# Performance work log

Hardware: AMD Instinct MI355X
Metric: run time of the kernel (lower is better)

The kernel has to match this reference:

```python
import jax, jax.numpy as jnp
from jax import lax
import numpy as np

N_BINS = 8
SIGMA = (1.0, 2.0)
ALPHA = (1.0, 2.0, 4.0)
BETA = (0.02, 0.05)
KSIZE = 7
BOUNDS = (0.0, 1.0)
C, H, W = 3, 512, 512


def gaussian_kernel(size, s):
    # matches torch: linspace(-size//2+1, size//2, size) == arange(size)-size//2 for odd size
    x = jnp.arange(size, dtype=jnp.float32) - size // 2
    g = jnp.exp(-(x[:, None] ** 2 + x[None, :] ** 2) / (2.0 * s ** 2))
    return g / jnp.sum(g)


def setup_inputs() -> dict:
    key = jax.random.key(0)
    im_th = jax.random.uniform(key, (H, W, C), dtype=jnp.float32)
    sks = max(3, int(SIGMA[-1] * 4))
    if sks % 2 == 0:
        sks += 1
    sigma_kernels = jnp.stack([gaussian_kernel(sks, s) for s in SIGMA])      # (S, Ks, Ks)
    alpha_kernels = jnp.stack([gaussian_kernel(KSIZE, a) for a in ALPHA])    # (A, k, k)
    edges = jnp.linspace(BOUNDS[0], BOUNDS[1], N_BINS + 1, dtype=jnp.float32)
    bin_centers = (edges[1:] + edges[:-1]) / 2.0                             # (N,)
    betas = jnp.array(BETA, dtype=jnp.float32)                               # (B,)
    return dict(im_th=im_th, sigma_kernels=sigma_kernels,
                alpha_kernels=alpha_kernels, bin_centers=bin_centers, betas=betas)


def _conv_per_channel(x, k):
    # x: (M, H, W); k: (K, kh, kw) -> (M, K, H, W). Channels treated as batch,
    # equivalent to torch grouped conv with groups=M and K kernels per group.
    p = k.shape[-1] // 2
    return lax.conv_general_dilated(x[:, None], k[:, None], (1, 1),
                                    [(p, p), (p, p)],
                                    dimension_numbers=('NCHW', 'OIHW', 'NCHW'))


def reference(im_th, sigma_kernels, alpha_kernels, bin_centers, betas):
    x = jnp.clip(im_th, 0.0, 1.0).transpose(2, 0, 1)  # (C, H, W)
    C_, H_, W_ = x.shape
    S = sigma_kernels.shape[0]
    A = alpha_kernels.shape[0]
    B = betas.shape[0]
    N = bin_centers.shape[0]
    # per-channel blur at each sigma: (C, S, H, W)
    conv = _conv_per_channel(x, sigma_kernels)
    # gaussian soft-binning: (B, N, C, S, H, W)
    diff = conv[None, None] - bin_centers[None, :, None, None, None, None]
    bv = betas[:, None, None, None, None, None]
    iso = jnp.exp(-0.5 * (diff / bv) ** 2) / (jnp.sqrt(2.0 * jnp.pi) * bv)
    # depthwise alpha aggregation over all B*N*C*S channels: (M, A, H, W)
    out = _conv_per_channel(iso.reshape(B * N * C_ * S, H_, W_), alpha_kernels)
    loi = out.reshape(B, N, C_, S, A, H_, W_).transpose(4, 0, 3, 2, 5, 6, 1)
    return loi  # (A, B, S, C, H, W, N)
```

## Files before the change

### kernel.cpp

```cpp
#include <hip/hip_runtime.h>

#define IMH 512
#define IMW 512

#define SM_OFF   0
#define IMT_OFF  560
#define SVT_OFF  1616
#define ISO_OFF  560
#define VV_OFF   4816

__global__ __launch_bounds__(256) void loi_fused(
    const float* __restrict__ im,
    const float* __restrict__ sigk,
    const float* __restrict__ alphak,
    const float* __restrict__ binc,
    const float* __restrict__ betas,
    float* __restrict__ out)
{
  const int t     = threadIdx.x;
  const int combo = blockIdx.z;
  const int b     = combo / 6;
  const int sc    = combo % 6;
  const int s     = sc / 3;
  const int c     = sc % 3;
  const int tx0   = blockIdx.x * 32;
  const int ty0   = blockIdx.y * 8;

  __shared__ __align__(16) float smem[12112];
  __shared__ float kf[3][8];
  __shared__ float sf[12];

  float* imt = smem + IMT_OFF;
  float* svt = smem + SVT_OFF;
  float* smt = smem + SM_OFF;

  for (int e = t; e < 1056; e += 256) {
    int j = e / 48, i = e - j * 48;
    float v = 0.f;
    if (i < 46) {
      int gy = ty0 + j - 7, gx = tx0 + i - 7;
      if (gy >= 0 && gy < IMH && gx >= 0 && gx < IMW) {
        v = im[(gy * IMW + gx) * 3 + c];
        v = fminf(fmaxf(v, 0.f), 1.f);
      }
    }
    imt[e] = v;
  }
  if (t < 9) {
    float acc = 0.f;
    #pragma unroll
    for (int j = 0; j < 9; j++) acc += sigk[s * 81 + t * 9 + j];
    sf[t] = acc;
  }
  if (t >= 32 && t < 56) {
    int a = (t - 32) >> 3, d = t & 7;
    float v = 0.f;
    if (d < 7) {
      #pragma unroll
      for (int j = 0; j < 7; j++) v += alphak[a * 49 + d * 7 + j];
    }
    kf[a][d] = v;
  }
  __syncthreads();

  for (int e = t; e < 672; e += 256) {
    int rr = e / 48, i = e - rr * 48;
    if (i < 46) {
      float acc = 0.f;
      #pragma unroll
      for (int d = 0; d < 9; d++) acc = fmaf(sf[d], imt[(rr + d) * 48 + i], acc);
      svt[e] = acc;
    }
  }
  __syncthreads();

  for (int e = t; e < 560; e += 256) {
    int rr = e / 40, j = e - rr * 40;
    if (j < 38) {
      float acc = 0.f;
      #pragma unroll
      for (int d = 0; d < 9; d++) acc = fmaf(sf[d], svt[rr * 48 + j + d], acc);
      smt[e] = acc;
    }
  }
  __syncthreads();

  const float beta = betas[b];
  const float norm = 0.39894228040143268f / beta;
  const float c2   = -0.72134752044448170f / (beta * beta);
  const float ctr  = binc[t & 7];
  float* iso = smem + ISO_OFF;
  for (int e = t; e < 4256; e += 256) {
    int q  = e >> 3;
    int rr = q / 38, jj = q - rr * 38;
    float v  = smt[rr * 40 + jj];
    float tt = v - ctr;
    float E  = exp2f(tt * tt * c2) * norm;
    int X = tx0 + jj - 3, Y = ty0 + rr - 3;
    bool valid = ((unsigned)X < IMW) && ((unsigned)Y < IMH);
    iso[e] = valid ? E : 0.f;
  }
  __syncthreads();

  float k0[7], k1[7], k2[7];
  #pragma unroll
  for (int d = 0; d < 7; d++) {
    k0[d] = kf[0][d];
    k1[d] = kf[1][d];
    k2[d] = kf[2][d];
  }

  float* vv = smem + VV_OFF;
  for (int g = t; g < 608; g += 256) {
    int ng = g & 1;
    int h  = g >> 1;
    int yr = h / 38, jj = h - yr * 38;
    int base = yr * 304 + jj * 8 + ng * 4;
    float a0x = 0.f, a0y = 0.f, a0z = 0.f, a0w = 0.f;
    float a1x = 0.f, a1y = 0.f, a1z = 0.f, a1w = 0.f;
    float a2x = 0.f, a2y = 0.f, a2z = 0.f, a2w = 0.f;
    #pragma unroll
    for (int d = 0; d < 7; d++) {
      float4 w = *(const float4*)&iso[base + d * 304];
      a0x = fmaf(k0[d], w.x, a0x); a0y = fmaf(k0[d], w.y, a0y);
      a0z = fmaf(k0[d], w.z, a0z); a0w = fmaf(k0[d], w.w, a0w);
      a1x = fmaf(k1[d], w.x, a1x); a1y = fmaf(k1[d], w.y, a1y);
      a1z = fmaf(k1[d], w.z, a1z); a1w = fmaf(k1[d], w.w, a1w);
      a2x = fmaf(k2[d], w.x, a2x); a2y = fmaf(k2[d], w.y, a2y);
      a2z = fmaf(k2[d], w.z, a2z); a2w = fmaf(k2[d], w.w, a2w);
    }
    *(float4*)&vv[base]        = make_float4(a0x, a0y, a0z, a0w);
    *(float4*)&vv[base + 2432] = make_float4(a1x, a1y, a1z, a1w);
    *(float4*)&vv[base + 4864] = make_float4(a2x, a2y, a2z, a2w);
  }
  __syncthreads();

  {
    const int col = t & 31;
    const int ng  = (t >> 5) & 1;
    const int rg  = t >> 6;
    const int gx  = tx0 + col;
    const float* vb = vv + col * 8 + ng * 4;
    #pragma unroll
    for (int rowi = 0; rowi < 2; rowi++) {
      const int row = rg * 2 + rowi;
      const float* vr = vb + row * 304;
      const size_t pb = (((size_t)(ty0 + row) * 512 + gx) << 3) + ng * 4;
      float* op = out + ((size_t)combo << 21) + pb;
      {
        float ax = 0.f, ay = 0.f, az = 0.f, aw = 0.f;
        #pragma unroll
        for (int d = 0; d < 7; d++) {
          float4 w = *(const float4*)(vr + d * 8);
          ax = fmaf(k0[d], w.x, ax); ay = fmaf(k0[d], w.y, ay);
          az = fmaf(k0[d], w.z, az); aw = fmaf(k0[d], w.w, aw);
        }
        *(float4*)op = make_float4(ax, ay, az, aw);
      }
      {
        float ax = 0.f, ay = 0.f, az = 0.f, aw = 0.f;
        #pragma unroll
        for (int d = 0; d < 7; d++) {
          float4 w = *(const float4*)(vr + 2432 + d * 8);
          ax = fmaf(k1[d], w.x, ax); ay = fmaf(k1[d], w.y, ay);
          az = fmaf(k1[d], w.z, az); aw = fmaf(k1[d], w.w, aw);
        }
        *(float4*)(op + ((size_t)12 << 21)) = make_float4(ax, ay, az, aw);
      }
      {
        float ax = 0.f, ay = 0.f, az = 0.f, aw = 0.f;
        #pragma unroll
        for (int d = 0; d < 7; d++) {
          float4 w = *(const float4*)(vr + 4864 + d * 8);
          ax = fmaf(k2[d], w.x, ax); ay = fmaf(k2[d], w.y, ay);
          az = fmaf(k2[d], w.z, az); aw = fmaf(k2[d], w.w, aw);
        }
        *(float4*)(op + ((size_t)24 << 21)) = make_float4(ax, ay, az, aw);
      }
    }
  }
}

extern "C" void kernel_launch(void* const* d_in, const int* in_sizes, int n_in,
                              void* d_out, int out_size, void* d_ws, size_t ws_size,
                              hipStream_t stream)
{
  const float* im   = (const float*)d_in[0];
  const float* sigk = (const float*)d_in[1];
  const float* alpk = (const float*)d_in[2];
  const float* binc = (const float*)d_in[3];
  const float* bets = (const float*)d_in[4];
  float* out = (float*)d_out;

  loi_fused<<<dim3(16, 64, 12), 256, 0, stream>>>(im, sigk, alpk, binc, bets, out);
}
```

Measured before the change: 367.9 us.

## Store soft-bin and vertical blur intermediates in fp16 and use packed half FMA

Stores the Gaussian soft-binning values and the vertical alpha-blur intermediates in shared memory as fp16, and computes both separable alpha-convolution passes with packed __hfma2 math. Each thread now handles two bins per exp pass and a full output pixel (8 bins) in the final pass. Launch bounds ask for 6 blocks per CU. The aim is to cut LDS footprint and bandwidth and double FMA throughput so occupancy rises, but fp16 accumulation lowers precision and may hurt accuracy against the fp32 reference. The output writes stay fp32, so a store-bound kernel may see little change.

```diff
diff --git a/kernel.cpp b/kernel.cpp
--- a/kernel.cpp
+++ b/kernel.cpp
@@ -1,15 +1,18 @@
 #include <hip/hip_runtime.h>
+#include <hip/hip_fp16.h>
 
 #define IMH 512
 #define IMW 512
 
-#define SM_OFF   0
-#define IMT_OFF  560
-#define SVT_OFF  1616
-#define ISO_OFF  560
-#define VV_OFF   4816
-
-__global__ __launch_bounds__(256) void loi_fused(
+
+__device__ __forceinline__ __half2 bc_h2(int v) {
+  union { int i; __half2 h; } u; u.i = v; return u.h;
+}
+__device__ __forceinline__ int bc_i(__half2 v) {
+  union { int i; __half2 h; } u; u.h = v; return u.i;
+}
+
+__global__ __launch_bounds__(256, 6) void loi_fused(
     const float* __restrict__ im,
     const float* __restrict__ sigk,
     const float* __restrict__ alphak,
@@ -26,13 +29,15 @@
   const int tx0   = blockIdx.x * 32;
   const int ty0   = blockIdx.y * 8;
 
-  __shared__ __align__(16) float smem[12112];
+  __shared__ __align__(16) float smt[560];
+  __shared__ __align__(16) unsigned char uni[23104];
   __shared__ float kf[3][8];
   __shared__ float sf[12];
 
-  float* imt = smem + IMT_OFF;
-  float* svt = smem + SVT_OFF;
-  float* smt = smem + SM_OFF;
+  float*  imt = (float*)uni;
+  float*  svt = (float*)(uni + 4224);
+  __half* iso = (__half*)uni;
+  __half* vv  = (__half*)(uni + 8512);
 
   for (int e = t; e < 1056; e += 256) {
     int j = e / 48, i = e - j * 48;
@@ -88,96 +93,99 @@
   const float beta = betas[b];
   const float norm = 0.39894228040143268f / beta;
   const float c2   = -0.72134752044448170f / (beta * beta);
-  const float ctr  = binc[t & 7];
-  float* iso = smem + ISO_OFF;
-  for (int e = t; e < 4256; e += 256) {
-    int q  = e >> 3;
+  const int   np   = t & 3;
+  const float ctr0 = binc[2 * np];
+  const float ctr1 = binc[2 * np + 1];
+  for (int u = t; u < 2128; u += 256) {
+    int q  = u >> 2;
     int rr = q / 38, jj = q - rr * 38;
     float v  = smt[rr * 40 + jj];
-    float tt = v - ctr;
-    float E  = exp2f(tt * tt * c2) * norm;
+    float t0 = v - ctr0, t1 = v - ctr1;
+    float E0 = exp2f(t0 * t0 * c2) * norm;
+    float E1 = exp2f(t1 * t1 * c2) * norm;
     int X = tx0 + jj - 3, Y = ty0 + rr - 3;
-    bool valid = ((unsigned)X < IMW) && ((unsigned)Y < IMH);
-    iso[e] = valid ? E : 0.f;
-  }
-  __syncthreads();
-
-  float k0[7], k1[7], k2[7];
+    if (!(((unsigned)X < IMW) && ((unsigned)Y < IMH))) { E0 = 0.f; E1 = 0.f; }
+    *(__half2*)(iso + q * 8 + np * 2) = __floats2half2_rn(E0, E1);
+  }
+  __syncthreads();
+
+  __half2 kh[3][7];
   #pragma unroll
-  for (int d = 0; d < 7; d++) {
-    k0[d] = kf[0][d];
-    k1[d] = kf[1][d];
-    k2[d] = kf[2][d];
-  }
-
-  float* vv = smem + VV_OFF;
-  for (int g = t; g < 608; g += 256) {
-    int ng = g & 1;
-    int h  = g >> 1;
-    int yr = h / 38, jj = h - yr * 38;
-    int base = yr * 304 + jj * 8 + ng * 4;
-    float a0x = 0.f, a0y = 0.f, a0z = 0.f, a0w = 0.f;
-    float a1x = 0.f, a1y = 0.f, a1z = 0.f, a1w = 0.f;
-    float a2x = 0.f, a2y = 0.f, a2z = 0.f, a2w = 0.f;
+  for (int a = 0; a < 3; a++)
+    #pragma unroll
+    for (int d = 0; d < 7; d++) kh[a][d] = __float2half2_rn(kf[a][d]);
+
+  for (int g = t; g < 304; g += 256) {
+    int yr = g / 38, jj = g - yr * 38;
+    const int base = yr * 38 + jj;
+    __half2 acc[3][4];
+    #pragma unroll
+    for (int a = 0; a < 3; a++)
+      #pragma unroll
+      for (int q = 0; q < 4; q++) acc[a][q] = __floats2half2_rn(0.f, 0.f);
     #pragma unroll
     for (int d = 0; d < 7; d++) {
-      float4 w = *(const float4*)&iso[base + d * 304];
-      a0x = fmaf(k0[d], w.x, a0x); a0y = fmaf(k0[d], w.y, a0y);
-      a0z = fmaf(k0[d], w.z, a0z); a0w = fmaf(k0[d], w.w, a0w);
-      a1x = fmaf(k1[d], w.x, a1x); a1y = fmaf(k1[d], w.y, a1y);
-      a1z = fmaf(k1[d], w.z, a1z); a1w = fmaf(k1[d], w.w, a1w);
-      a2x = fmaf(k2[d], w.x, a2x); a2y = fmaf(k2[d], w.y, a2y);
-      a2z = fmaf(k2[d], w.z, a2z); a2w = fmaf(k2[d], w.w, a2w);
-    }
-    *(float4*)&vv[base]        = make_float4(a0x, a0y, a0z, a0w);
-    *(float4*)&vv[base + 2432] = make_float4(a1x, a1y, a1z, a1w);
-    *(float4*)&vv[base + 4864] = make_float4(a2x, a2y, a2z, a2w);
-  }
-  __syncthreads();
-
-  {
-    const int col = t & 31;
-    const int ng  = (t >> 5) & 1;
-    const int rg  = t >> 6;
-    const int gx  = tx0 + col;
-    const float* vb = vv + col * 8 + ng * 4;
-    #pragma unroll
-    for (int rowi = 0; rowi < 2; rowi++) {
-      const int row = rg * 2 + rowi;
-      const float* vr = vb + row * 304;
-      const size_t pb = (((size_t)(ty0 + row) * 512 + gx) << 3) + ng * 4;
-      float* op = out + ((size_t)combo << 21) + pb;
-      {
-        float ax = 0.f, ay = 0.f, az = 0.f, aw = 0.f;
-        #pragma unroll
-        for (int d = 0; d < 7; d++) {
-          float4 w = *(const float4*)(vr + d * 8);
-          ax = fmaf(k0[d], w.x, ax); ay = fmaf(k0[d], w.y, ay);
-          az = fmaf(k0[d], w.z, az); aw = fmaf(k0[d], w.w, aw);
-        }
-        *(float4*)op = make_float4(ax, ay, az, aw);
+      int4 raw = *(const int4*)(iso + ((base + d * 38) << 3));
+      __half2 w0 = bc_h2(raw.x), w1 = bc_h2(raw.y);
+      __half2 w2 = bc_h2(raw.z), w3 = bc_h2(raw.w);
+      #pragma unroll
+      for (int a = 0; a < 3; a++) {
+        acc[a][0] = __hfma2(kh[a][d], w0, acc[a][0]);
+        acc[a][1] = __hfma2(kh[a][d], w1, acc[a][1]);
+        acc[a][2] = __hfma2(kh[a][d], w2, acc[a][2]);
+        acc[a][3] = __hfma2(kh[a][d], w3, acc[a][3]);
       }
-      {
-        float ax = 0.f, ay = 0.f, az = 0.f, aw = 0.f;
-        #pragma unroll
-        for (int d = 0; d < 7; d++) {
-          float4 w = *(const float4*)(vr + 2432 + d * 8);
-          ax = fmaf(k1[d], w.x, ax); ay = fmaf(k1[d], w.y, ay);
-          az = fmaf(k1[d], w.z, az); aw = fmaf(k1[d], w.w, aw);
-        }
-        *(float4*)(op + ((size_t)12 << 21)) = make_float4(ax, ay, az, aw);
+    }
+    #pragma unroll
+    for (int a = 0; a < 3; a++) {
+      int4 o;
+      o.x = bc_i(acc[a][0]); o.y = bc_i(acc[a][1]);
+      o.z = bc_i(acc[a][2]); o.w = bc_i(acc[a][3]);
+      *(int4*)(vv + ((((a << 3) + yr) * 38 + jj) << 3)) = o;
+    }
+  }
+  __syncthreads();
+
+  const int col = t & 31;
+  const int row = t >> 5;
+  float* op = out + ((size_t)combo << 21)
+                  + ((size_t)(ty0 + row) * 512 + (tx0 + col)) * 8;
+  #pragma unroll
+  for (int a = 0; a < 3; a++) {
+    const int base = ((a << 3) + row) * 38 + col;
+    __half2 pA0, pA1, pA2, pA3, pB0, pB1, pB2, pB3;
+    {
+      int4 r0 = *(const int4*)(vv + (base << 3));
+      pA0 = __hmul2(kh[a][0], bc_h2(r0.x)); pA1 = __hmul2(kh[a][0], bc_h2(r0.y));
+      pA2 = __hmul2(kh[a][0], bc_h2(r0.z)); pA3 = __hmul2(kh[a][0], bc_h2(r0.w));
+      int4 r1 = *(const int4*)(vv + ((base + 1) << 3));
+      pB0 = __hmul2(kh[a][1], bc_h2(r1.x)); pB1 = __hmul2(kh[a][1], bc_h2(r1.y));
+      pB2 = __hmul2(kh[a][1], bc_h2(r1.z)); pB3 = __hmul2(kh[a][1], bc_h2(r1.w));
+    }
+    #pragma unroll
+    for (int d = 2; d < 7; d += 2) {
+      int4 rA = *(const int4*)(vv + ((base + d) << 3));
+      pA0 = __hfma2(kh[a][d], bc_h2(rA.x), pA0);
+      pA1 = __hfma2(kh[a][d], bc_h2(rA.y), pA1);
+      pA2 = __hfma2(kh[a][d], bc_h2(rA.z), pA2);
+      pA3 = __hfma2(kh[a][d], bc_h2(rA.w), pA3);
+      if (d + 1 < 7) {
+        int4 rB = *(const int4*)(vv + ((base + d + 1) << 3));
+        pB0 = __hfma2(kh[a][d + 1], bc_h2(rB.x), pB0);
+        pB1 = __hfma2(kh[a][d + 1], bc_h2(rB.y), pB1);
+        pB2 = __hfma2(kh[a][d + 1], bc_h2(rB.z), pB2);
+        pB3 = __hfma2(kh[a][d + 1], bc_h2(rB.w), pB3);
       }
-      {
-        float ax = 0.f, ay = 0.f, az = 0.f, aw = 0.f;
-        #pragma unroll
-        for (int d = 0; d < 7; d++) {
-          float4 w = *(const float4*)(vr + 4864 + d * 8);
-          ax = fmaf(k2[d], w.x, ax); ay = fmaf(k2[d], w.y, ay);
-          az = fmaf(k2[d], w.z, az); aw = fmaf(k2[d], w.w, aw);
-        }
-        *(float4*)(op + ((size_t)24 << 21)) = make_float4(ax, ay, az, aw);
-      }
-    }
+    }
+    float2 a0 = __half22float2(pA0), b0 = __half22float2(pB0);
+    float2 a1 = __half22float2(pA1), b1 = __half22float2(pB1);
+    float2 a2 = __half22float2(pA2), b2 = __half22float2(pB2);
+    float2 a3 = __half22float2(pA3), b3 = __half22float2(pB3);
+    float4 lo = make_float4(a0.x + b0.x, a0.y + b0.y, a1.x + b1.x, a1.y + b1.y);
+    float4 hi = make_float4(a2.x + b2.x, a2.y + b2.y, a3.x + b3.x, a3.y + b3.y);
+    float* p = op + ((size_t)(a * 12) << 21);
+    *(float4*)p       = lo;
+    *(float4*)(p + 4) = hi;
   }
 }
 
```

Measured after the change: 324.8 us. -11.7%, faster.
